# Optimization experiments

Hardware: AMD Instinct MI355X
Metric: run time of the kernel (lower is better)

Reference implementation:

```python
import jax, jax.numpy as jnp
import numpy as np

B, S, D = 4, 1024, 2048
NH, HD = 16, 128  # nhead, head_dim
SCALE = HD ** -0.5


def setup_inputs() -> dict:
    key = jax.random.key(0)
    ks = jax.random.split(key, 7)
    query = jax.random.normal(ks[0], (B, S, D), dtype=jnp.float32)
    key_t = jax.random.normal(ks[1], (B, S, D), dtype=jnp.float32)
    value = jax.random.normal(ks[2], (B, S, D), dtype=jnp.float32)
    # qkv_proj: Linear(D, 3D) with bias; out_proj: Linear(D, D) with bias
    Wqkv = jax.random.normal(ks[3], (3 * D, D), dtype=jnp.float32) * (D ** -0.5)
    bqkv = jnp.zeros((3 * D,), dtype=jnp.float32)
    Wout = jax.random.normal(ks[4], (D, D), dtype=jnp.float32) * (D ** -0.5)
    bout = jnp.zeros((D,), dtype=jnp.float32)
    return {"query": query, "key": key_t, "value": value,
            "Wqkv": Wqkv, "bqkv": bqkv, "Wout": Wout, "bout": bout}


def reference(query, key, value, Wqkv, bqkv, Wout, bout):
    # NOTE: module ignores `key`/`value` args; qkv comes from query alone.
    b, s, d = query.shape
    qkv = query @ Wqkv.T + bqkv                       # (B,S,3D)
    q, k, v = jnp.split(qkv, 3, axis=-1)
    q = q.reshape(b, s, NH, HD).transpose(0, 2, 1, 3) * SCALE  # (B,H,S,hd)
    k = k.reshape(b, s, NH, HD).transpose(0, 2, 1, 3)          # (B,H,S,hd)
    # faithful replication of the module's odd v permutation:
    v = v.reshape(b, s, HD, NH).transpose(0, 2, 1, 3)          # (B,hd,S,H)
    v = v.reshape(b, s, NH * HD).reshape(b, s, NH, HD).transpose(0, 2, 1, 3)  # (B,H,S,hd)
    scores = jnp.einsum('bhqd,bhkd->bhqk', q, k)               # (B,H,S,S)
    causal = jnp.triu(jnp.ones((s, s), dtype=bool), k=1)
    scores = jnp.where(causal, -jnp.inf, scores)
    attn = jax.nn.softmax(scores.astype(jnp.float32), axis=-1).astype(query.dtype)
    out = jnp.einsum('bhqk,bhkd->bhqd', attn, v)               # (B,H,S,hd)
    out = out.transpose(0, 2, 1, 3).reshape(b, s, d)
    return out @ Wout.T + bout
```

## Files before the change

kernel.cpp:

```cpp
#include <hip/hip_runtime.h>
#include <hip/hip_bf16.h>
#include <stdint.h>

typedef __bf16 bf16x8 __attribute__((ext_vector_type(8)));
typedef float  floatx4 __attribute__((ext_vector_type(4)));

#define NEG_BIG (-1e30f)

#define GLD16(g, l) __builtin_amdgcn_global_load_lds(                         \
    (__attribute__((address_space(1))) void*)(g),                             \
    (__attribute__((address_space(3))) void*)(l), 16, 0, 0)

__device__ __forceinline__ void cvt16(const float* __restrict__ s,
                                      __hip_bfloat16* __restrict__ d) {
    float4 f[4];
#pragma unroll
    for (int i = 0; i < 4; i++) f[i] = ((const float4*)s)[i];
    union { __hip_bfloat16 h[16]; uint4 u[2]; } o;
#pragma unroll
    for (int i = 0; i < 4; i++) {
        o.h[4 * i + 0] = __float2bfloat16(f[i].x);
        o.h[4 * i + 1] = __float2bfloat16(f[i].y);
        o.h[4 * i + 2] = __float2bfloat16(f[i].z);
        o.h[4 * i + 3] = __float2bfloat16(f[i].w);
    }
    ((uint4*)d)[0] = o.u[0];
    ((uint4*)d)[1] = o.u[1];
}

__global__ __launch_bounds__(256)
void cvt3_f32_bf16(const float* __restrict__ a, size_t na8,
                   const float* __restrict__ b, size_t nb8,
                   const float* __restrict__ c, size_t nc8,
                   __hip_bfloat16* __restrict__ da,
                   __hip_bfloat16* __restrict__ db,
                   __hip_bfloat16* __restrict__ dc)
{
    const size_t total  = na8 + nb8 + nc8;
    const size_t stride = (size_t)gridDim.x * blockDim.x;
    for (size_t idx = (size_t)blockIdx.x * blockDim.x + threadIdx.x;
         idx < total; idx += stride) {
        const float* s; __hip_bfloat16* d; size_t o;
        if (idx < na8)            { s = a; d = da; o = idx; }
        else if (idx < na8 + nb8) { s = b; d = db; o = idx - na8; }
        else                      { s = c; d = dc; o = idx - na8 - nb8; }
        const float4 f0 = ((const float4*)s)[o * 2 + 0];
        const float4 f1 = ((const float4*)s)[o * 2 + 1];
        union { __hip_bfloat16 h[8]; uint4 u; } z;
        z.h[0] = __float2bfloat16(f0.x); z.h[1] = __float2bfloat16(f0.y);
        z.h[2] = __float2bfloat16(f0.z); z.h[3] = __float2bfloat16(f0.w);
        z.h[4] = __float2bfloat16(f1.x); z.h[5] = __float2bfloat16(f1.y);
        z.h[6] = __float2bfloat16(f1.z); z.h[7] = __float2bfloat16(f1.w);
        ((uint4*)d)[o] = z.u;
    }
}

template <bool OUT_F32>
__global__ __launch_bounds__(512, 2)
void gemm256_nt_bias(const __hip_bfloat16* __restrict__ A,
                     const __hip_bfloat16* __restrict__ B,
                     const float* __restrict__ bias, void* __restrict__ Cv,
                     int M, int N, int K, int lda, int ldb, int nbx)
{
    __shared__ __align__(16) __hip_bfloat16 Asm[2][256 * 64];
    __shared__ __align__(16) __hip_bfloat16 Bsm[2][256 * 64];

    const int nwg = gridDim.x, cpx = nwg >> 3;
    const int flat = blockIdx.x;
    const int swz  = (flat & 7) * cpx + (flat >> 3);
    const int bx = swz % nbx, by = swz / nbx;
    const int m0 = by * 256, n0 = bx * 256;

    const int t    = threadIdx.x;
    const int wave = t >> 6, lane = t & 63;
    const int quad = lane >> 4, l16 = lane & 15;
    const int wr   = wave >> 2, wc = wave & 3;
    const int NT   = K >> 6;

    const int s_   = wave >> 2;
    const int w3   = wave & 3;
    const int l8   = lane >> 3;
    const int g_   = (lane & 7) ^ l8;
    const __hip_bfloat16* aSrc = A + (size_t)(m0 + s_ * 128 + w3 * 8 + l8) * lda + g_ * 8;
    const __hip_bfloat16* bSrc = B + (size_t)(n0 + wave * 8 + l8) * ldb + g_ * 8;

    auto stageA = [&](int tk, int b, int buf) {
        GLD16(aSrc + (size_t)(b * 32) * lda + tk * 64,
              &Asm[buf][0] + (s_ * 128 + b * 32 + w3 * 8) * 64);
    };
    auto stageBhalf = [&](int tk, int h, int buf) {
#pragma unroll
        for (int j = 0; j < 2; j++)
            GLD16(bSrc + (size_t)(h * 128 + j * 64) * ldb + tk * 64,
                  &Bsm[buf][0] + (h * 128 + j * 64 + wave * 8) * 64);
    };

    const int g0 = (quad ^ (l16 & 7)) << 3;

    floatx4 acc[8][4];
    const floatx4 zero = {0.f, 0.f, 0.f, 0.f};
#pragma unroll
    for (int mi = 0; mi < 8; mi++)
#pragma unroll
        for (int ni = 0; ni < 4; ni++) acc[mi][ni] = zero;

    stageA(0, 0, 0); stageA(0, 1, 0); stageA(0, 2, 0); stageA(0, 3, 0);
    stageBhalf(0, 0, 0); stageBhalf(0, 1, 0);
    if (NT > 1) {
        stageA(1, 0, 1); stageA(1, 1, 1); stageA(1, 2, 1);
        asm volatile("s_waitcnt vmcnt(3)" ::: "memory");
    } else {
        asm volatile("s_waitcnt vmcnt(0)" ::: "memory");
    }
    __syncthreads();

    bf16x8 bfr[4][2];
    int cb = 0;
    for (int tk = 0; tk < NT; ++tk, cb ^= 1) {
        const __hip_bfloat16* Ab = &Asm[cb][0];
        const __hip_bfloat16* Bb = &Bsm[cb][0];
        const int nb = cb ^ 1;

#pragma unroll
        for (int p = 0; p < 4; p++) {
            bf16x8 af[2][2];
#pragma unroll
            for (int i = 0; i < 2; i++)
#pragma unroll
                for (int ks = 0; ks < 2; ks++)
                    af[i][ks] = *(const bf16x8*)(
                        Ab + (wr * 128 + (2 * p + i) * 16 + l16) * 64 +
                        (g0 ^ (ks ? 32 : 0)));
            if (p == 0) {
#pragma unroll
                for (int ni = 0; ni < 4; ni++)
#pragma unroll
                    for (int ks = 0; ks < 2; ks++)
                        bfr[ni][ks] = *(const bf16x8*)(
                            Bb + (wc * 64 + ni * 16 + l16) * 64 +
                            (g0 ^ (ks ? 32 : 0)));
            }
            if (p == 0) {
                if (tk + 1 < NT) { stageA(tk + 1, 3, nb); stageBhalf(tk + 1, 0, nb); }
            } else if (p == 1) {
                if (tk + 1 < NT) stageBhalf(tk + 1, 1, nb);
                if (tk + 2 < NT) stageA(tk + 2, 0, cb);
            } else if (p == 2) {
                if (tk + 2 < NT) stageA(tk + 2, 1, cb);
            } else {
                if (tk + 2 < NT) stageA(tk + 2, 2, cb);
            }

            __builtin_amdgcn_s_barrier();
            asm volatile("s_waitcnt lgkmcnt(0)" ::: "memory");
            __builtin_amdgcn_s_setprio(1);
#pragma unroll
            for (int ks = 0; ks < 2; ks++)
#pragma unroll
                for (int i = 0; i < 2; i++)
#pragma unroll
                    for (int ni = 0; ni < 4; ni++)
                        acc[2 * p + i][ni] = __builtin_amdgcn_mfma_f32_16x16x32_bf16(
                            af[i][ks], bfr[ni][ks], acc[2 * p + i][ni], 0, 0, 0);
            __builtin_amdgcn_s_setprio(0);
            if (p == 3) {
                if (tk + 2 < NT)
                    asm volatile("s_waitcnt vmcnt(3)" ::: "memory");
                else if (tk + 1 < NT)
                    asm volatile("s_waitcnt vmcnt(0)" ::: "memory");
            }
            __builtin_amdgcn_s_barrier();
        }
    }

#pragma unroll
    for (int mi = 0; mi < 8; mi++) {
        const int row = m0 + wr * 128 + mi * 16 + quad * 4;
#pragma unroll
        for (int ni = 0; ni < 4; ni++) {
            const int col = n0 + wc * 64 + ni * 16 + l16;
            const float bv = bias[col];
#pragma unroll
            for (int r = 0; r < 4; r++) {
                const float v = acc[mi][ni][r] + bv;
                if (OUT_F32)
                    ((float*)Cv)[(size_t)(row + r) * N + col] = v;
                else
                    ((__hip_bfloat16*)Cv)[(size_t)(row + r) * N + col] =
                        __float2bfloat16(v);
            }
        }
    }
}

template <bool A_F32, bool B_F32, bool OUT_F32>
__global__ __launch_bounds__(256, 2)
void gemm_nt_bias(const void* __restrict__ Av, const void* __restrict__ Bv,
                  const float* __restrict__ bias, void* __restrict__ Cv,
                  int M, int N, int K, int lda, int ldb)
{
    __shared__ __align__(16) __hip_bfloat16 Asm[128 * 32];
    __shared__ __align__(16) __hip_bfloat16 Bsm[128 * 32];
    const int m0   = blockIdx.y * 128;
    const int n0   = blockIdx.x * 128;
    const int t    = threadIdx.x;
    const int wave = t >> 6, lane = t & 63;
    const int quad = lane >> 4, l16 = lane & 15;
    const int wr   = wave >> 1, wc = wave & 1;

    floatx4 zero = {0.f, 0.f, 0.f, 0.f};
    floatx4 acc[4][4];
    for (int i = 0; i < 4; i++)
        for (int j = 0; j < 4; j++) acc[i][j] = zero;

    for (int k0 = 0; k0 < K; k0 += 32) {
        if (A_F32) {
            const float* A = (const float*)Av;
            const int row = t >> 1, half = t & 1;
            cvt16(A + (size_t)(m0 + row) * lda + k0 + half * 16,
                  Asm + row * 32 + half * 16);
        } else {
            const __hip_bfloat16* A = (const __hip_bfloat16*)Av;
            for (int j = 0; j < 2; ++j) {
                const int chunk = (wave * 2 + j) * 64 + lane;
                const int row   = chunk >> 2;
                const int kc    = chunk & 3;
                GLD16(A + (size_t)(m0 + row) * lda + k0 + kc * 8,
                      Asm + (wave * 2 + j) * 512);
            }
        }
        if (B_F32) {
            const float* B = (const float*)Bv;
            const int row = t >> 1, half = t & 1;
            cvt16(B + (size_t)(n0 + row) * ldb + k0 + half * 16,
                  Bsm + row * 32 + half * 16);
        } else {
            const __hip_bfloat16* B = (const __hip_bfloat16*)Bv;
            for (int j = 0; j < 2; ++j) {
                const int chunk = (wave * 2 + j) * 64 + lane;
                const int row   = chunk >> 2;
                const int kc    = chunk & 3;
                GLD16(B + (size_t)(n0 + row) * ldb + k0 + kc * 8,
                      Bsm + (wave * 2 + j) * 512);
            }
        }
        __syncthreads();

        bf16x8 af[4], bf[4];
        for (int i = 0; i < 4; i++) {
            af[i] = *(const bf16x8*)(Asm + (wr * 64 + i * 16 + l16) * 32 + quad * 8);
            bf[i] = *(const bf16x8*)(Bsm + (wc * 64 + i * 16 + l16) * 32 + quad * 8);
        }
        for (int mi = 0; mi < 4; mi++)
            for (int ni = 0; ni < 4; ni++)
                acc[mi][ni] = __builtin_amdgcn_mfma_f32_16x16x32_bf16(
                    af[mi], bf[ni], acc[mi][ni], 0, 0, 0);
        __syncthreads();
    }

    for (int mi = 0; mi < 4; mi++) {
        const int row = m0 + wr * 64 + mi * 16 + quad * 4;
        for (int ni = 0; ni < 4; ni++) {
            const int col = n0 + wc * 64 + ni * 16 + l16;
            const float bv = bias[col];
            for (int r = 0; r < 4; r++) {
                const float v = acc[mi][ni][r] + bv;
                if (OUT_F32)
                    ((float*)Cv)[(size_t)(row + r) * N + col] = v;
                else
                    ((__hip_bfloat16*)Cv)[(size_t)(row + r) * N + col] =
                        __float2bfloat16(v);
            }
        }
    }
}

__global__ __launch_bounds__(256)
void permute_v(const __hip_bfloat16* __restrict__ QKV,
               __hip_bfloat16* __restrict__ Vpt)
{
    __shared__ __align__(16) __hip_bfloat16 S[64 * 64];
    const int blk = blockIdx.x;
    const int sb = blk & 31, h = (blk >> 5) & 15, b = blk >> 9;
    const int t = threadIdx.x;

    for (int j = 0; j < 2; j++) {
        const int chunk = j * 256 + t;
        const int lrow  = chunk >> 3;
        const int lcol  = (chunk & 7) * 8;
        const int r8 = lrow >> 3, jj = lrow & 7;
        const int srow = r8 * 128 + h * 8 + jj;
        const int scol = sb * 64 + lcol;
        *(uint4*)(S + chunk * 8) =
            *(const uint4*)(QKV + ((size_t)(b * 1024) + srow) * 6144 + 4096 + scol);
    }
    __syncthreads();

    const size_t obase = (((size_t)(b * 16 + h)) * 32 + sb) * 4096;
    for (int i = 0; i < 16; i++) {
        const int lin = t + 256 * i;
        const int hd = lin >> 5, ss = lin & 31;
        Vpt[obase + lin] =
            S[((ss & 7) * 8 + (hd >> 4)) * 64 + (ss >> 3) * 16 + (hd & 15)];
    }
}

__global__ __launch_bounds__(256, 2)
void flash_attn(const __hip_bfloat16* __restrict__ QKV,
                const __hip_bfloat16* __restrict__ Vpt,
                __hip_bfloat16* __restrict__ O)
{
    __shared__ __align__(16) __hip_bfloat16 Kt[2][64 * 128];
    __shared__ __align__(16) __hip_bfloat16 Vt[2][2 * 128 * 32];
    __shared__ __align__(16) __hip_bfloat16 Pl[64 * 64];

    const int bid  = blockIdx.x;
    const int pair = bid >> 6;
    const int g    = bid & 63;
    const int b    = g >> 4, h = g & 15;
    const int t    = threadIdx.x;
    const int wave = t >> 6, lane = t & 63;
    const int quad = lane >> 4, l16 = lane & 15;
    const float scale = 0.08838834764831845f;

    const int    rowb  = b * 1024;
    const size_t vbase = (((size_t)(b * 16 + h)) * 32) * 4096;
    const floatx4 zero = {0.f, 0.f, 0.f, 0.f};

    auto stageK = [&](int tk, int bufi) {
        const int kv0 = tk * 64;
        __hip_bfloat16* dst = &Kt[bufi][0];
#pragma unroll
        for (int j = 0; j < 4; j++) {
            const int c0 = (wave * 4 + j) * 64 + lane;
            const int r  = c0 >> 4;
            const int gg = (c0 & 15) ^ (r & 7);
            GLD16(QKV + ((size_t)(rowb + kv0 + r)) * 6144 + 2048 + h * 128 + gg * 8,
                  dst + (wave * 4 + j) * 512);
        }
    };
    auto stageV = [&](int tk, int bufi) {
        const __hip_bfloat16* src = Vpt + vbase + (size_t)(tk * 2) * 4096;
        __hip_bfloat16* dst = &Vt[bufi][0];
#pragma unroll
        for (int j = 0; j < 4; j++) {
            const int c0   = (wave * 4 + j) * 64 + lane;
            const int half = c0 >> 9, w = c0 & 511;
            const int r    = w >> 2;
            const int gg   = (w & 3) ^ (r & 3);
            GLD16(src + half * 4096 + r * 32 + gg * 8,
                  dst + (wave * 4 + j) * 512);
        }
    };

    for (int ph = 0; ph < 2; ++ph) {
        const int qb = ph ? (15 - pair) * 64 : pair * 64;
        const int nt = ph ? 16 - pair       : pair + 1;

        bf16x8 qf[4];
        {
            const size_t rb = ((size_t)(rowb + qb + wave * 16 + l16)) * 6144 + h * 128;
#pragma unroll
            for (int kc = 0; kc < 4; kc++)
                qf[kc] = *(const bf16x8*)(QKV + rb + kc * 32 + quad * 8);
        }

        float m_i[4], l_i[4];
        floatx4 oacc[8];
#pragma unroll
        for (int r = 0; r < 4; r++) { m_i[r] = NEG_BIG; l_i[r] = 0.f; }
#pragma unroll
        for (int ni = 0; ni < 8; ni++) oacc[ni] = zero;

        stageK(0, 0); stageV(0, 0);

        for (int tk = 0; tk < nt; ++tk) {
            const int cur = tk & 1;
            if (tk + 1 < nt) {
                stageK(tk + 1, cur ^ 1); stageV(tk + 1, cur ^ 1);
                asm volatile("s_waitcnt vmcnt(8)" ::: "memory");
            } else {
                asm volatile("s_waitcnt vmcnt(0)" ::: "memory");
            }
            __builtin_amdgcn_s_barrier();
            asm volatile("" ::: "memory");

            const __hip_bfloat16* Kb = &Kt[cur][0];
            const __hip_bfloat16* Vb = &Vt[cur][0];
            const int kv0 = tk * 64;

            floatx4 sc[4];
#pragma unroll
            for (int cbk = 0; cbk < 4; cbk++) {
                floatx4 s = zero;
                const int r  = cbk * 16 + l16;
                const int sw = r & 7;
#pragma unroll
                for (int kc = 0; kc < 4; kc++) {
                    bf16x8 kf = *(const bf16x8*)(
                        Kb + r * 128 + (((kc * 4 + quad) ^ sw) << 3));
                    s = __builtin_amdgcn_mfma_f32_16x16x32_bf16(qf[kc], kf, s, 0, 0, 0);
                }
                sc[cbk] = s;
            }

            const int qrow = qb + wave * 16 + quad * 4;
            if (tk == nt - 1) {
#pragma unroll
                for (int rr = 0; rr < 4; rr++)
#pragma unroll
                    for (int cbk = 0; cbk < 4; cbk++) {
                        const int col = kv0 + cbk * 16 + l16;
                        const float v = sc[cbk][rr] * scale;
                        sc[cbk][rr] = (col > qrow + rr) ? NEG_BIG : v;
                    }
            } else {
#pragma unroll
                for (int rr = 0; rr < 4; rr++)
#pragma unroll
                    for (int cbk = 0; cbk < 4; cbk++) sc[cbk][rr] *= scale;
            }
            float mx[4];
#pragma unroll
            for (int rr = 0; rr < 4; rr++)
                mx[rr] = fmaxf(fmaxf(sc[0][rr], sc[1][rr]),
                               fmaxf(sc[2][rr], sc[3][rr]));
#pragma unroll
            for (int off = 1; off < 16; off <<= 1)
#pragma unroll
                for (int rr = 0; rr < 4; rr++)
                    mx[rr] = fmaxf(mx[rr], __shfl_xor(mx[rr], off));

            float alpha[4], rsum[4];
#pragma unroll
            for (int rr = 0; rr < 4; rr++) {
                const float mnew = fmaxf(m_i[rr], mx[rr]);
                alpha[rr] = __expf(m_i[rr] - mnew);
                m_i[rr] = mnew;
                float acc = 0.f;
#pragma unroll
                for (int cbk = 0; cbk < 4; cbk++) {
                    const float pv = __expf(sc[cbk][rr] - mnew);
                    sc[cbk][rr] = pv;
                    acc += pv;
                }
                rsum[rr] = acc;
            }
#pragma unroll
            for (int off = 1; off < 16; off <<= 1)
#pragma unroll
                for (int rr = 0; rr < 4; rr++)
                    rsum[rr] += __shfl_xor(rsum[rr], off);
#pragma unroll
            for (int rr = 0; rr < 4; rr++)
                l_i[rr] = l_i[rr] * alpha[rr] + rsum[rr];
#pragma unroll
            for (int ni = 0; ni < 8; ni++)
#pragma unroll
                for (int rr = 0; rr < 4; rr++) oacc[ni][rr] *= alpha[rr];

#pragma unroll
            for (int cbk = 0; cbk < 4; cbk++)
#pragma unroll
                for (int rr = 0; rr < 4; rr++) {
                    const int row = wave * 16 + quad * 4 + rr;
                    const int col = cbk * 16 + l16;
                    Pl[row * 64 + ((((col >> 3) ^ (row & 7)) << 3) | (col & 7))] =
                        __float2bfloat16(sc[cbk][rr]);
                }
            asm volatile("s_waitcnt lgkmcnt(0)" ::: "memory");

            const int prow = wave * 16 + l16;
            bf16x8 pf[2];
#pragma unroll
            for (int kc = 0; kc < 2; kc++)
                pf[kc] = *(const bf16x8*)(
                    Pl + prow * 64 + (((kc * 4 + quad) ^ (prow & 7)) << 3));
#pragma unroll
            for (int ni = 0; ni < 8; ni++) {
                const int vr = ni * 16 + l16;
#pragma unroll
                for (int kc = 0; kc < 2; kc++) {
                    bf16x8 vf = *(const bf16x8*)(
                        Vb + kc * 4096 + vr * 32 + (((quad ^ (vr & 3))) << 3));
                    oacc[ni] = __builtin_amdgcn_mfma_f32_16x16x32_bf16(
                        pf[kc], vf, oacc[ni], 0, 0, 0);
                }
            }

            asm volatile("" ::: "memory");
            __builtin_amdgcn_s_barrier();
            asm volatile("" ::: "memory");
        }

        float inv[4];
#pragma unroll
        for (int rr = 0; rr < 4; rr++) inv[rr] = 1.0f / l_i[rr];
#pragma unroll
        for (int ni = 0; ni < 8; ni++)
#pragma unroll
            for (int rr = 0; rr < 4; rr++) {
                const int row = qb + wave * 16 + quad * 4 + rr;
                O[((size_t)rowb + row) * 6144 + 4096 + h * 128 + ni * 16 + l16] =
                    __float2bfloat16(oacc[ni][rr] * inv[rr]);
            }
    }
}

extern "C" void kernel_launch(void* const* d_in, const int* in_sizes, int n_in,
                              void* d_out, int out_size, void* d_ws, size_t ws_size,
                              hipStream_t stream) {
    const float* query = (const float*)d_in[0];
    const float* Wqkv = (const float*)d_in[3];
    const float* bqkv = (const float*)d_in[4];
    const float* Wout = (const float*)d_in[5];
    const float* bout = (const float*)d_in[6];
    float* out = (float*)d_out;

    const size_t MB = 1048576;
    char* ws = (char*)d_ws;
    __hip_bfloat16* QKV = (__hip_bfloat16*)ws;
    __hip_bfloat16* Vpt = (__hip_bfloat16*)(ws + 48 * MB);
    __hip_bfloat16* Att = QKV + 4096;

    dim3 blk(256);

    if (ws_size >= 113 * MB) {
        __hip_bfloat16* Qbf     = (__hip_bfloat16*)(ws + 64 * MB);
        __hip_bfloat16* Wqkv_bf = (__hip_bfloat16*)(ws + 80 * MB);
        __hip_bfloat16* Wout_bf = (__hip_bfloat16*)(ws + 104 * MB);

        cvt3_f32_bf16<<<dim3(2048), blk, 0, stream>>>(
            query, (size_t)4096 * 2048 / 8,
            Wqkv,  (size_t)6144 * 2048 / 8,
            Wout,  (size_t)2048 * 2048 / 8,
            Qbf, Wqkv_bf, Wout_bf);
        gemm256_nt_bias<false><<<dim3(384), dim3(512), 0, stream>>>(
            Qbf, Wqkv_bf, bqkv, QKV, 4096, 6144, 2048, 2048, 2048, 24);
        permute_v<<<dim3(2048), blk, 0, stream>>>(QKV, Vpt);
        flash_attn<<<dim3(512), blk, 0, stream>>>(QKV, Vpt, QKV);
        gemm_nt_bias<false, false, true><<<dim3(16, 32), blk, 0, stream>>>(
            Att, Wout_bf, bout, out, 4096, 2048, 2048, 6144, 2048);
    } else {
        gemm_nt_bias<true, true, false><<<dim3(48, 32), blk, 0, stream>>>(
            query, Wqkv, bqkv, QKV, 4096, 6144, 2048, 2048, 2048);
        permute_v<<<dim3(2048), blk, 0, stream>>>(QKV, Vpt);
        flash_attn<<<dim3(512), blk, 0, stream>>>(QKV, Vpt, QKV);
        gemm_nt_bias<false, true, true><<<dim3(16, 32), blk, 0, stream>>>(
            Att, Wout, bout, out, 4096, 2048, 2048, 6144, 2048);
    }
}
```

Measured before the change: 388.6 us.

## Shrink QKV GEMM tile to 128x256 and reuse it for the output projection

The 256x256 8-wave GEMM becomes a 128x256 tile with a two-phase pipelined K loop. The QKV projection launches 768 workgroups instead of 384. The output projection now uses the same 8-wave kernel instead of the older 256-thread gemm_nt_bias. The smaller tile gives more workgroups for better CU load balance and halves the A-tile LDS, at the cost of lower arithmetic intensity per tile and more B reloads.

```diff
diff --git a/kernel.cpp b/kernel.cpp
--- a/kernel.cpp
+++ b/kernel.cpp
@@ -57,19 +57,19 @@
 
 template <bool OUT_F32>
 __global__ __launch_bounds__(512, 2)
-void gemm256_nt_bias(const __hip_bfloat16* __restrict__ A,
-                     const __hip_bfloat16* __restrict__ B,
-                     const float* __restrict__ bias, void* __restrict__ Cv,
-                     int M, int N, int K, int lda, int ldb, int nbx)
+void gemm8p_nt_bias(const __hip_bfloat16* __restrict__ A,
+                    const __hip_bfloat16* __restrict__ B,
+                    const float* __restrict__ bias, void* __restrict__ Cv,
+                    int M, int N, int K, int lda, int ldb, int nby)
 {
-    __shared__ __align__(16) __hip_bfloat16 Asm[2][256 * 64];
+    __shared__ __align__(16) __hip_bfloat16 Asm[2][128 * 64];
     __shared__ __align__(16) __hip_bfloat16 Bsm[2][256 * 64];
 
     const int nwg = gridDim.x, cpx = nwg >> 3;
     const int flat = blockIdx.x;
     const int swz  = (flat & 7) * cpx + (flat >> 3);
-    const int bx = swz % nbx, by = swz / nbx;
-    const int m0 = by * 256, n0 = bx * 256;
+    const int by = swz % nby, bx = swz / nby;
+    const int m0 = by * 128, n0 = bx * 256;
 
     const int t    = threadIdx.x;
     const int wave = t >> 6, lane = t & 63;
@@ -77,105 +77,106 @@
     const int wr   = wave >> 2, wc = wave & 3;
     const int NT   = K >> 6;
 
-    const int s_   = wave >> 2;
-    const int w3   = wave & 3;
-    const int l8   = lane >> 3;
-    const int g_   = (lane & 7) ^ l8;
-    const __hip_bfloat16* aSrc = A + (size_t)(m0 + s_ * 128 + w3 * 8 + l8) * lda + g_ * 8;
-    const __hip_bfloat16* bSrc = B + (size_t)(n0 + wave * 8 + l8) * ldb + g_ * 8;
-
-    auto stageA = [&](int tk, int b, int buf) {
-        GLD16(aSrc + (size_t)(b * 32) * lda + tk * 64,
-              &Asm[buf][0] + (s_ * 128 + b * 32 + w3 * 8) * 64);
+    const int l8 = lane >> 3;
+    const int g_ = (lane & 7) ^ l8;
+    const int aRowBase = (wave >> 2) * 64 + (wave & 3) * 8;
+    const int bRowBase = wave * 8;
+
+    auto stageA = [&](int tk, int j, int buf) {
+        GLD16(A + (size_t)(m0 + aRowBase + j * 32 + l8) * lda + tk * 64 + g_ * 8,
+              &Asm[buf][0] + (aRowBase + j * 32) * 64);
     };
-    auto stageBhalf = [&](int tk, int h, int buf) {
-#pragma unroll
-        for (int j = 0; j < 2; j++)
-            GLD16(bSrc + (size_t)(h * 128 + j * 64) * ldb + tk * 64,
-                  &Bsm[buf][0] + (h * 128 + j * 64 + wave * 8) * 64);
+    auto stageB = [&](int tk, int j, int buf) {
+        GLD16(B + (size_t)(n0 + bRowBase + j * 64 + l8) * ldb + tk * 64 + g_ * 8,
+              &Bsm[buf][0] + (bRowBase + j * 64) * 64);
     };
 
     const int g0 = (quad ^ (l16 & 7)) << 3;
 
-    floatx4 acc[8][4];
+    floatx4 acc[4][4];
     const floatx4 zero = {0.f, 0.f, 0.f, 0.f};
 #pragma unroll
-    for (int mi = 0; mi < 8; mi++)
+    for (int mi = 0; mi < 4; mi++)
 #pragma unroll
         for (int ni = 0; ni < 4; ni++) acc[mi][ni] = zero;
 
-    stageA(0, 0, 0); stageA(0, 1, 0); stageA(0, 2, 0); stageA(0, 3, 0);
-    stageBhalf(0, 0, 0); stageBhalf(0, 1, 0);
+    stageA(0, 0, 0); stageA(0, 1, 0);
+    stageB(0, 0, 0); stageB(0, 1, 0); stageB(0, 2, 0); stageB(0, 3, 0);
     if (NT > 1) {
-        stageA(1, 0, 1); stageA(1, 1, 1); stageA(1, 2, 1);
+        stageA(1, 0, 1); stageB(1, 0, 1); stageB(1, 1, 1);
         asm volatile("s_waitcnt vmcnt(3)" ::: "memory");
     } else {
         asm volatile("s_waitcnt vmcnt(0)" ::: "memory");
     }
     __syncthreads();
 
-    bf16x8 bfr[4][2];
     int cb = 0;
     for (int tk = 0; tk < NT; ++tk, cb ^= 1) {
         const __hip_bfloat16* Ab = &Asm[cb][0];
         const __hip_bfloat16* Bb = &Bsm[cb][0];
         const int nb = cb ^ 1;
 
-#pragma unroll
-        for (int p = 0; p < 4; p++) {
-            bf16x8 af[2][2];
+        bf16x8 af[2][2], bfr[4][2];
+#pragma unroll
+        for (int i = 0; i < 2; i++)
+#pragma unroll
+            for (int ks = 0; ks < 2; ks++)
+                af[i][ks] = *(const bf16x8*)(
+                    Ab + (wr * 64 + i * 16 + l16) * 64 + (g0 ^ (ks ? 32 : 0)));
+#pragma unroll
+        for (int ni = 0; ni < 4; ni++)
+#pragma unroll
+            for (int ks = 0; ks < 2; ks++)
+                bfr[ni][ks] = *(const bf16x8*)(
+                    Bb + (wc * 64 + ni * 16 + l16) * 64 + (g0 ^ (ks ? 32 : 0)));
+        if (tk + 1 < NT) {
+            stageA(tk + 1, 1, nb); stageB(tk + 1, 2, nb); stageB(tk + 1, 3, nb);
+        }
+        __builtin_amdgcn_s_barrier();
+        asm volatile("s_waitcnt lgkmcnt(0)" ::: "memory");
+        __builtin_amdgcn_s_setprio(1);
+#pragma unroll
+        for (int ks = 0; ks < 2; ks++)
 #pragma unroll
             for (int i = 0; i < 2; i++)
 #pragma unroll
-                for (int ks = 0; ks < 2; ks++)
-                    af[i][ks] = *(const bf16x8*)(
-                        Ab + (wr * 128 + (2 * p + i) * 16 + l16) * 64 +
-                        (g0 ^ (ks ? 32 : 0)));
-            if (p == 0) {
-#pragma unroll
                 for (int ni = 0; ni < 4; ni++)
-#pragma unroll
-                    for (int ks = 0; ks < 2; ks++)
-                        bfr[ni][ks] = *(const bf16x8*)(
-                            Bb + (wc * 64 + ni * 16 + l16) * 64 +
-                            (g0 ^ (ks ? 32 : 0)));
-            }
-            if (p == 0) {
-                if (tk + 1 < NT) { stageA(tk + 1, 3, nb); stageBhalf(tk + 1, 0, nb); }
-            } else if (p == 1) {
-                if (tk + 1 < NT) stageBhalf(tk + 1, 1, nb);
-                if (tk + 2 < NT) stageA(tk + 2, 0, cb);
-            } else if (p == 2) {
-                if (tk + 2 < NT) stageA(tk + 2, 1, cb);
-            } else {
-                if (tk + 2 < NT) stageA(tk + 2, 2, cb);
-            }
-
-            __builtin_amdgcn_s_barrier();
-            asm volatile("s_waitcnt lgkmcnt(0)" ::: "memory");
-            __builtin_amdgcn_s_setprio(1);
+                    acc[i][ni] = __builtin_amdgcn_mfma_f32_16x16x32_bf16(
+                        af[i][ks], bfr[ni][ks], acc[i][ni], 0, 0, 0);
+        __builtin_amdgcn_s_setprio(0);
+        __builtin_amdgcn_s_barrier();
+
+#pragma unroll
+        for (int i = 0; i < 2; i++)
 #pragma unroll
             for (int ks = 0; ks < 2; ks++)
-#pragma unroll
-                for (int i = 0; i < 2; i++)
-#pragma unroll
-                    for (int ni = 0; ni < 4; ni++)
-                        acc[2 * p + i][ni] = __builtin_amdgcn_mfma_f32_16x16x32_bf16(
-                            af[i][ks], bfr[ni][ks], acc[2 * p + i][ni], 0, 0, 0);
-            __builtin_amdgcn_s_setprio(0);
-            if (p == 3) {
-                if (tk + 2 < NT)
-                    asm volatile("s_waitcnt vmcnt(3)" ::: "memory");
-                else if (tk + 1 < NT)
-                    asm volatile("s_waitcnt vmcnt(0)" ::: "memory");
-            }
-            __builtin_amdgcn_s_barrier();
-        }
-    }
-
-#pragma unroll
-    for (int mi = 0; mi < 8; mi++) {
-        const int row = m0 + wr * 128 + mi * 16 + quad * 4;
+                af[i][ks] = *(const bf16x8*)(
+                    Ab + (wr * 64 + (2 + i) * 16 + l16) * 64 + (g0 ^ (ks ? 32 : 0)));
+        if (tk + 2 < NT) {
+            stageA(tk + 2, 0, cb); stageB(tk + 2, 0, cb); stageB(tk + 2, 1, cb);
+        }
+        __builtin_amdgcn_s_barrier();
+        asm volatile("s_waitcnt lgkmcnt(0)" ::: "memory");
+        __builtin_amdgcn_s_setprio(1);
+#pragma unroll
+        for (int ks = 0; ks < 2; ks++)
+#pragma unroll
+            for (int i = 0; i < 2; i++)
+#pragma unroll
+                for (int ni = 0; ni < 4; ni++)
+                    acc[2 + i][ni] = __builtin_amdgcn_mfma_f32_16x16x32_bf16(
+                        af[i][ks], bfr[ni][ks], acc[2 + i][ni], 0, 0, 0);
+        __builtin_amdgcn_s_setprio(0);
+        if (tk + 2 < NT)
+            asm volatile("s_waitcnt vmcnt(3)" ::: "memory");
+        else if (tk + 1 < NT)
+            asm volatile("s_waitcnt vmcnt(0)" ::: "memory");
+        __builtin_amdgcn_s_barrier();
+    }
+
+#pragma unroll
+    for (int mi = 0; mi < 4; mi++) {
+        const int row = m0 + wr * 64 + mi * 16 + quad * 4;
 #pragma unroll
         for (int ni = 0; ni < 4; ni++) {
             const int col = n0 + wc * 64 + ni * 16 + l16;
@@ -535,12 +536,12 @@
             Wqkv,  (size_t)6144 * 2048 / 8,
             Wout,  (size_t)2048 * 2048 / 8,
             Qbf, Wqkv_bf, Wout_bf);
-        gemm256_nt_bias<false><<<dim3(384), dim3(512), 0, stream>>>(
-            Qbf, Wqkv_bf, bqkv, QKV, 4096, 6144, 2048, 2048, 2048, 24);
+        gemm8p_nt_bias<false><<<dim3(768), dim3(512), 0, stream>>>(
+            Qbf, Wqkv_bf, bqkv, QKV, 4096, 6144, 2048, 2048, 2048, 32);
         permute_v<<<dim3(2048), blk, 0, stream>>>(QKV, Vpt);
         flash_attn<<<dim3(512), blk, 0, stream>>>(QKV, Vpt, QKV);
-        gemm_nt_bias<false, false, true><<<dim3(16, 32), blk, 0, stream>>>(
-            Att, Wout_bf, bout, out, 4096, 2048, 2048, 6144, 2048);
+        gemm8p_nt_bias<true><<<dim3(256), dim3(512), 0, stream>>>(
+            Att, Wout_bf, bout, out, 4096, 2048, 2048, 6144, 2048, 32);
     } else {
         gemm_nt_bias<true, true, false><<<dim3(48, 32), blk, 0, stream>>>(
             query, Wqkv, bqkv, QKV, 4096, 6144, 2048, 2048, 2048);
```

New measurement: 381.1 us. Within noise of the previous version (-1.9%).
